# Kernel optimization log

Hardware: AMD Instinct MI355X
Metric: run time of the kernel (lower is better)

Reference implementation:

```python
import jax, jax.numpy as jnp
import numpy as np

GAMMA = 2.0
EPS = 1e-06
LAMBDA_DISTANCE = 1.0
LAMBDA_NORMAL = 0.01
LAMBDA_LAPLACIAN = 0.1
CLS = 1


def vertex_normals(v, f, eps=EPS):
    # v: [N,3], f: [F,3] int. Scatter face normals to vertices, then normalize.
    fv = v[f]  # [F,3,3]
    fn = jnp.cross(fv[:, 1] - fv[:, 0], fv[:, 2] - fv[:, 0])  # [F,3]
    vn = jnp.zeros_like(v)
    vn = vn.at[f[:, 0]].add(fn).at[f[:, 1]].add(fn).at[f[:, 2]].add(fn)
    norm = jnp.maximum(jnp.linalg.norm(vn, axis=-1, keepdims=True), eps)
    return vn / norm


def squared_cdist(a, b):
    # [Na,3] x [Nb,3] -> squared euclidean distances [Na,Nb] (clamped >= 0)
    a2 = jnp.sum(a * a, axis=1)[:, None]
    b2 = jnp.sum(b * b, axis=1)[None, :]
    d2 = a2 + b2 - 2.0 * (a @ b.T)
    return jnp.maximum(d2, 0.0)


def sample_binary_targets(label, v, cls=CLS):
    # Nearest-neighbor grid_sample, align_corners=True, padding zeros.
    # grid = 2*v - 1 -> voxel index = round(v * (size-1)); v[:,0]->W, v[:,1]->H, v[:,2]->D.
    D, H, W = label.shape[2], label.shape[3], label.shape[4]
    ix = jnp.round(v[:, 0] * (W - 1)).astype(jnp.int32)
    iy = jnp.round(v[:, 1] * (H - 1)).astype(jnp.int32)
    iz = jnp.round(v[:, 2] * (D - 1)).astype(jnp.int32)
    inb = (ix >= 0) & (ix < W) & (iy >= 0) & (iy < H) & (iz >= 0) & (iz < D)
    ixc = jnp.clip(ix, 0, W - 1)
    iyc = jnp.clip(iy, 0, H - 1)
    izc = jnp.clip(iz, 0, D - 1)
    vals = (label[0, 0, izc, iyc, ixc] == cls).astype(jnp.float32)
    return jnp.where(inb, vals, 0.0)


def spatial_consistency_loss(rel_pos, targets, gamma=GAMMA, eps=EPS):
    p = jnp.clip(rel_pos, eps, 1.0 - eps)
    pos = targets > 0.5
    pc = jnp.sum(pos).astype(p.dtype)
    tot = jnp.asarray(p.shape[0], p.dtype)
    nc = tot - pc
    alpha = nc / (tot + eps)
    lpos = -alpha * jnp.power(1.0 - p, gamma) * jnp.log(p)
    lneg = -(1.0 - alpha) * jnp.power(p, gamma) * jnp.log(1.0 - p)
    return jnp.sum(jnp.where(pos, lpos, lneg)) / (tot + eps)


def laplacian_uniform(v, f):
    # Uniform mesh Laplacian smoothing: || mean(neighbors) - v ||, averaged.
    i = jnp.concatenate([f[:, 0], f[:, 1], f[:, 2], f[:, 1], f[:, 2], f[:, 0]])
    j = jnp.concatenate([f[:, 1], f[:, 2], f[:, 0], f[:, 0], f[:, 1], f[:, 2]])
    nsum = jnp.zeros_like(v).at[i].add(v[j])
    deg = jnp.zeros((v.shape[0],), v.dtype).at[i].add(1.0)
    lap = nsum / jnp.maximum(deg, 1.0)[:, None] - v
    return jnp.mean(jnp.linalg.norm(lap, axis=1))


def loss_forward(pred_vertices, relative_positions, gt_vertices, pred_faces, gt_faces, label):
    gt_v = jax.lax.stop_gradient(gt_vertices)  # gt comes from label volume; detached in original
    gt_normals = vertex_normals(gt_v, gt_faces)
    # spatial (focal-style) loss
    targets = sample_binary_targets(label, pred_vertices)
    spatial = spatial_consistency_loss(relative_positions, targets)
    # chamfer-style squared surface distance
    d2 = squared_cdist(pred_vertices, gt_v)  # [Np,Ng]
    distance = jnp.mean(jnp.min(d2, axis=1)) + jnp.mean(jnp.min(d2, axis=0))
    # normal consistency vs nearest gt vertex
    pred_normals = vertex_normals(pred_vertices, pred_faces)
    nearest = jnp.argmin(d2, axis=1)
    normal = jnp.mean((pred_normals - gt_normals[nearest]) ** 2)
    # uniform laplacian smoothing
    laplacian = laplacian_uniform(pred_vertices, pred_faces)
    total = spatial + LAMBDA_DISTANCE * distance + LAMBDA_NORMAL * normal + LAMBDA_LAPLACIAN * laplacian
    return total


def setup_inputs() -> dict:
    key = jax.random.key(0)
    k1, k2, k3, k4, k5, k6 = jax.random.split(key, 6)
    Np, Ng = 8192, 12000
    pred_vertices = jax.random.uniform(k1, (Np, 3), dtype=jnp.float32)
    relative_positions = jax.random.uniform(k2, (Np,), dtype=jnp.float32)
    gt_vertices = jax.random.uniform(k3, (Ng, 3), dtype=jnp.float32)
    pred_faces = jax.random.randint(k4, (2 * Np, 3), 0, Np, dtype=jnp.int32)
    gt_faces = jax.random.randint(k5, (2 * Ng, 3), 0, Ng, dtype=jnp.int32)
    label = jax.random.randint(k6, (1, 1, 96, 96, 96), 0, 2, dtype=jnp.int32)
    return {"pred_vertices": pred_vertices, "relative_positions": relative_positions,
            "gt_vertices": gt_vertices, "pred_faces": pred_faces,
            "gt_faces": gt_faces, "label": label}


def reference(pred_vertices, relative_positions, gt_vertices, pred_faces, gt_faces, label):
    return loss_forward(pred_vertices, relative_positions, gt_vertices, pred_faces, gt_faces, label)
```

## Files before the change

### kernel.cpp

```cpp
#include <hip/hip_runtime.h>
#include <math.h>

#define NP 8192
#define NG 12000
#define NFP 16384
#define NFG 24000
#define EPSF 1e-6f

#define GR 16
#define NC (GR*GR*GR)
#define HCELL 0.0625f
#define QL 16

#define FB ((NFG + NFP + 1023) / 1024)
#define D1_BLOCKS (2 + FB)

#define QPBLK 64
#define PQB (NP / QPBLK)
#define GQB ((NG + QPBLK - 1) / QPBLK)
#define D2_BLOCKS (PQB + GQB)

#define CAPP  4608
#define CWCAP 1312

#define FIN_BLOCKS (NP / 256)

static constexpr size_t OFF_STARTP = 0;
static constexpr size_t OFF_STARTG = 16640;
static constexpr size_t OFF_SORTP  = 33280;
static constexpr size_t OFF_SORTG  = 164352;
static constexpr size_t OFF_GTN    = 356352;
static constexpr size_t OFF_PNN    = 500352;
static constexpr size_t OFF_NSUM   = 598656;
static constexpr size_t OFF_DEG    = 696960;
static constexpr size_t OFF_NEAR   = 729728;
static constexpr size_t OFF_ACCUM  = 762496;
static constexpr size_t OFF_DONE   = 762528;
static constexpr size_t ZERO_BYTES = OFF_DONE + 4 - OFF_GTN;

__device__ __forceinline__ int cell_of(float x) {
    int c = (int)(x * (float)GR);
    return min(max(c, 0), GR - 1);
}

__device__ __forceinline__ void build_cells(const float* __restrict__ pts, int n,
                                            unsigned* __restrict__ start,
                                            float4* __restrict__ sorted,
                                            unsigned* h, unsigned* wsum) {
    int t = threadIdx.x;
    int lane = t & 63, wid = t >> 6;
    for (int i = t; i < NC; i += 1024) h[i] = 0u;
    __syncthreads();
    for (int i = t; i < n; i += 1024) {
        int c = (cell_of(pts[3*i+2]) * GR + cell_of(pts[3*i+1])) * GR + cell_of(pts[3*i]);
        atomicAdd(&h[c], 1u);
    }
    __syncthreads();
    unsigned a0 = h[4*t], a1 = h[4*t+1], a2 = h[4*t+2], a3 = h[4*t+3];
    unsigned tsum = a0 + a1 + a2 + a3;
    unsigned x = tsum;
    #pragma unroll
    for (int off = 1; off < 64; off <<= 1) {
        unsigned y = __shfl_up(x, off, 64);
        if (lane >= off) x += y;
    }
    if (lane == 63) wsum[wid] = x;
    __syncthreads();
    if (t < 16) {
        unsigned w = wsum[t];
        #pragma unroll
        for (int off = 1; off < 16; off <<= 1) {
            unsigned y = __shfl_up(w, off, 64);
            if (t >= off) w += y;
        }
        wsum[t] = w;
    }
    __syncthreads();
    unsigned base = (wid ? wsum[wid-1] : 0u) + (x - tsum);
    unsigned e0 = base, e1 = base + a0, e2 = base + a0 + a1, e3 = base + a0 + a1 + a2;
    start[4*t] = e0; start[4*t+1] = e1; start[4*t+2] = e2; start[4*t+3] = e3;
    h[4*t] = e0; h[4*t+1] = e1; h[4*t+2] = e2; h[4*t+3] = e3;
    __syncthreads();
    for (int i = t; i < n; i += 1024) {
        float px = pts[3*i], py = pts[3*i+1], pz = pts[3*i+2];
        int c = (cell_of(pz) * GR + cell_of(py)) * GR + cell_of(px);
        unsigned pos = atomicAdd(&h[c], 1u);
        sorted[pos] = make_float4(px, py, pz, __int_as_float(i));
    }
    if (t == 0) start[NC] = (unsigned)n;
}

__global__ __launch_bounds__(1024) void build_face_kernel(const float* __restrict__ pred,
                                                          const float* __restrict__ gt,
                                                          const int* __restrict__ pf,
                                                          const int* __restrict__ gf,
                                                          unsigned* __restrict__ startP,
                                                          unsigned* __restrict__ startG,
                                                          float4* __restrict__ sortP,
                                                          float4* __restrict__ sortG,
                                                          float* __restrict__ gtn,
                                                          float* __restrict__ pnn,
                                                          float* __restrict__ nsum,
                                                          float* __restrict__ deg) {
    __shared__ unsigned h[NC];
    __shared__ unsigned wsum[16];
    int b = blockIdx.x, t = threadIdx.x;
    if (b == 0) {
        build_cells(pred, NP, startP, sortP, h, wsum);
    } else if (b == 1) {
        build_cells(gt, NG, startG, sortG, h, wsum);
    } else {
        int f = (b - 2) * 1024 + t;
        if (f < NFG) {
            int i0 = gf[3*f], i1 = gf[3*f+1], i2 = gf[3*f+2];
            float ax = gt[3*i0], ay = gt[3*i0+1], az = gt[3*i0+2];
            float bx = gt[3*i1], by = gt[3*i1+1], bz = gt[3*i1+2];
            float cx = gt[3*i2], cy = gt[3*i2+1], cz = gt[3*i2+2];
            float ux = bx-ax, uy = by-ay, uz = bz-az;
            float wx = cx-ax, wy = cy-ay, wz = cz-az;
            float nx = uy*wz - uz*wy, ny = uz*wx - ux*wz, nz = ux*wy - uy*wx;
            atomicAdd(&gtn[3*i0+0], nx); atomicAdd(&gtn[3*i0+1], ny); atomicAdd(&gtn[3*i0+2], nz);
            atomicAdd(&gtn[3*i1+0], nx); atomicAdd(&gtn[3*i1+1], ny); atomicAdd(&gtn[3*i1+2], nz);
            atomicAdd(&gtn[3*i2+0], nx); atomicAdd(&gtn[3*i2+1], ny); atomicAdd(&gtn[3*i2+2], nz);
        } else if (f < NFG + NFP) {
            int u = f - NFG;
            int i0 = pf[3*u], i1 = pf[3*u+1], i2 = pf[3*u+2];
            float ax = pred[3*i0], ay = pred[3*i0+1], az = pred[3*i0+2];
            float bx = pred[3*i1], by = pred[3*i1+1], bz = pred[3*i1+2];
            float cx = pred[3*i2], cy = pred[3*i2+1], cz = pred[3*i2+2];
            float ux = bx-ax, uy = by-ay, uz = bz-az;
            float wx = cx-ax, wy = cy-ay, wz = cz-az;
            float nx = uy*wz - uz*wy, ny = uz*wx - ux*wz, nz = ux*wy - uy*wx;
            atomicAdd(&pnn[3*i0+0], nx); atomicAdd(&pnn[3*i0+1], ny); atomicAdd(&pnn[3*i0+2], nz);
            atomicAdd(&pnn[3*i1+0], nx); atomicAdd(&pnn[3*i1+1], ny); atomicAdd(&pnn[3*i1+2], nz);
            atomicAdd(&pnn[3*i2+0], nx); atomicAdd(&pnn[3*i2+1], ny); atomicAdd(&pnn[3*i2+2], nz);
            atomicAdd(&nsum[3*i0+0], bx+cx); atomicAdd(&nsum[3*i0+1], by+cy); atomicAdd(&nsum[3*i0+2], bz+cz);
            atomicAdd(&nsum[3*i1+0], cx+ax); atomicAdd(&nsum[3*i1+1], cy+ay); atomicAdd(&nsum[3*i1+2], cz+az);
            atomicAdd(&nsum[3*i2+0], ax+bx); atomicAdd(&nsum[3*i2+1], ay+by); atomicAdd(&nsum[3*i2+2], az+bz);
            atomicAdd(&deg[i0], 2.0f); atomicAdd(&deg[i1], 2.0f); atomicAdd(&deg[i2], 2.0f);
        }
    }
}

__device__ __forceinline__ float wave_sum(float x) {
    #pragma unroll
    for (int o = 32; o > 0; o >>= 1) x += __shfl_down(x, o, 64);
    return x;
}

__device__ __forceinline__ unsigned long long u64min(unsigned long long a,
                                                     unsigned long long b) {
    return a < b ? a : b;
}

__device__ __forceinline__ unsigned long long pack_key(float px, float py, float pz,
                                                       float4 q) {
    float ddx = px - q.x, ddy = py - q.y, ddz = pz - q.z;
    float d2 = fmaf(ddx, ddx, fmaf(ddy, ddy, ddz*ddz));
    return ((unsigned long long)__float_as_uint(d2) << 32) |
           (unsigned)__float_as_int(q.w);
}

__device__ unsigned long long group_nn(int lane, float px, float py, float pz,
                                       const float4* __restrict__ Sg,
                                       const unsigned* __restrict__ CSg,
                                       const float4* Sl, const unsigned* CSl,
                                       int c_lo, unsigned p_lo, bool staged) {
    int cx = cell_of(px), cy = cell_of(py), cz = cell_of(pz);
    unsigned long long best = 0xFFFFFFFFFFFFFFFFULL;
    {
        unsigned long long lb = 0xFFFFFFFFFFFFFFFFULL;
        for (int k = lane; k < 27; k += QL) {
            int z = cz + k / 9 - 1, y = cy + (k % 9) / 3 - 1, x = cx + k % 3 - 1;
            if (((unsigned)z < GR) & ((unsigned)y < GR) & ((unsigned)x < GR)) {
                int c = (z * GR + y) * GR + x;
                if (staged) {
                    unsigned s0 = CSl[c - c_lo];
                    unsigned s1 = CSl[c + 1 - c_lo];
                    for (unsigned u = s0; u < s1; ++u)
                        lb = u64min(lb, pack_key(px, py, pz, Sl[u - p_lo]));
                } else {
                    unsigned s0 = CSg[c];
                    unsigned s1 = CSg[c + 1];
                    for (unsigned u = s0; u < s1; ++u)
                        lb = u64min(lb, pack_key(px, py, pz, Sg[u]));
                }
            }
        }
        best = lb;
        #pragma unroll
        for (int m = 1; m < QL; m <<= 1)
            best = u64min(best, (unsigned long long)__shfl_xor((long long)best, m, 64));
        bool covered = (cx - 1 <= 0) & (cx + 1 >= GR - 1) &
                       (cy - 1 <= 0) & (cy + 1 >= GR - 1) &
                       (cz - 1 <= 0) & (cz + 1 >= GR - 1);
        float blo = 1.0e30f;
        if (cx - 1 > 0)      blo = fminf(blo, px - (float)(cx - 1) * HCELL);
        if (cx + 1 < GR - 1) blo = fminf(blo, (float)(cx + 2) * HCELL - px);
        if (cy - 1 > 0)      blo = fminf(blo, py - (float)(cy - 1) * HCELL);
        if (cy + 1 < GR - 1) blo = fminf(blo, (float)(cy + 2) * HCELL - py);
        if (cz - 1 > 0)      blo = fminf(blo, pz - (float)(cz - 1) * HCELL);
        if (cz + 1 < GR - 1) blo = fminf(blo, (float)(cz + 2) * HCELL - pz);
        float bd2 = __uint_as_float((unsigned)(best >> 32));
        if (covered || (bd2 <= blo * blo)) return best;
    }
    for (int r = 2; ; ++r) {
        int w = 2 * r + 1;
        int nrows = w * w;
        int x0 = max(cx - r, 0), x1 = min(cx + r, GR - 1);
        unsigned long long lb = 0xFFFFFFFFFFFFFFFFULL;
        for (int k = lane; k < nrows; k += QL) {
            int z = cz + k / w - r, y = cy + k % w - r;
            if (z >= 0 && z < GR && y >= 0 && y < GR) {
                int rowbase = (z * GR + y) * GR;
                unsigned s0 = CSg[rowbase + x0];
                unsigned s1 = CSg[rowbase + x1 + 1];
                for (unsigned u = s0; u < s1; ++u)
                    lb = u64min(lb, pack_key(px, py, pz, Sg[u]));
            }
        }
        best = u64min(best, lb);
        #pragma unroll
        for (int m = 1; m < QL; m <<= 1)
            best = u64min(best, (unsigned long long)__shfl_xor((long long)best, m, 64));
        bool covered = (cx - r <= 0) & (cx + r >= GR - 1) &
                       (cy - r <= 0) & (cy + r >= GR - 1) &
                       (cz - r <= 0) & (cz + r >= GR - 1);
        if (covered) break;
        float blo = 1.0e30f;
        if (cx - r > 0)      blo = fminf(blo, px - (float)(cx - r) * HCELL);
        if (cx + r < GR - 1) blo = fminf(blo, (float)(cx + r + 1) * HCELL - px);
        if (cy - r > 0)      blo = fminf(blo, py - (float)(cy - r) * HCELL);
        if (cy + r < GR - 1) blo = fminf(blo, (float)(cy + r + 1) * HCELL - py);
        if (cz - r > 0)      blo = fminf(blo, pz - (float)(cz - r) * HCELL);
        if (cz + r < GR - 1) blo = fminf(blo, (float)(cz + r + 1) * HCELL - pz);
        float bd2 = __uint_as_float((unsigned)(best >> 32));
        if (bd2 <= blo * blo) break;
    }
    return best;
}

__global__ __launch_bounds__(1024) void query_kernel(const float4* __restrict__ sortP,
                                                     const float4* __restrict__ sortG,
                                                     const unsigned* __restrict__ startP,
                                                     const unsigned* __restrict__ startG,
                                                     int* __restrict__ nearestIdx,
                                                     float* __restrict__ accum) {
    __shared__ float4 lpts[CAPP];
    __shared__ unsigned lcs[CWCAP];
    __shared__ float qacc;
    __shared__ int s_info[4];
    int b = blockIdx.x, t = threadIdx.x;

    bool is_pred = (b < PQB);
    const float4*   Q  = is_pred ? sortP  : sortG;
    const float4*   S  = is_pred ? sortG  : sortP;
    const unsigned* CS = is_pred ? startG : startP;
    int qbase = (is_pred ? b : (b - PQB)) * QPBLK;
    int nq = min(QPBLK, (is_pred ? NP : NG) - qbase);

    if (t == 0) {
        qacc = 0.0f;
        float4 qf = Q[qbase], ql = Q[qbase + nq - 1];
        int z_lo = cell_of(qf.z), z_hi = cell_of(ql.z);
        int c_lo  = max(z_lo - 1, 0) * (GR * GR);
        int c_end = min(z_hi + 2, GR) * (GR * GR);
        int cw = c_end - c_lo + 1;
        unsigned p_lo = CS[c_lo], p_hi = CS[c_end];
        int np = (int)(p_hi - p_lo);
        bool ok = (cw <= CWCAP) && (np <= CAPP);
        s_info[0] = c_lo; s_info[1] = (int)p_lo; s_info[2] = np;
        s_info[3] = ok ? cw : -cw;
    }
    __syncthreads();
    int c_lo = s_info[0];
    unsigned p_lo = (unsigned)s_info[1];
    int np = s_info[2];
    int cw = s_info[3];
    bool staged = (cw > 0);
    if (staged) {
        for (int i = t; i < np; i += 1024) lpts[i] = S[p_lo + i];
        for (int i = t; i < cw; i += 1024) lcs[i]  = CS[c_lo + i];
    }
    __syncthreads();

    int lane = t & (QL - 1), group = t >> 4;
    float r0 = 0.0f;
    if (group < nq) {
        int qid = qbase + group;
        float4 P = Q[qid];
        unsigned long long key = group_nn(lane, P.x, P.y, P.z, S, CS,
                                          lpts, lcs, c_lo, p_lo, staged);
        if (lane == 0) {
            r0 = __uint_as_float((unsigned)(key >> 32));
            if (is_pred)
                nearestIdx[__float_as_int(P.w)] = (int)(unsigned)(key & 0xffffffffu);
        }
    }
    r0 = wave_sum(r0);
    if ((t & 63) == 0) atomicAdd(&qacc, r0);
    __syncthreads();
    if (t == 0) atomicAdd(&accum[is_pred ? 0 : 6], qacc);
}

__global__ __launch_bounds__(256) void finish_kernel(const float* __restrict__ pred,
                                                     const float* __restrict__ relpos,
                                                     const int* __restrict__ label,
                                                     const float* __restrict__ pnn,
                                                     const float* __restrict__ gtn,
                                                     const float* __restrict__ nsum,
                                                     const float* __restrict__ deg,
                                                     const int* __restrict__ nearestIdx,
                                                     float* __restrict__ accum,
                                                     unsigned* __restrict__ done,
                                                     float* __restrict__ out) {
    int v = blockIdx.x * 256 + threadIdx.x;
    float px = pred[3*v], py = pred[3*v+1], pz = pred[3*v+2];
    int nearest = nearestIdx[v];

    float ax = pnn[3*v], ay = pnn[3*v+1], az = pnn[3*v+2];
    float an = fmaxf(sqrtf(ax*ax + ay*ay + az*az), EPSF);
    float gx = gtn[3*nearest], gy = gtn[3*nearest+1], gz = gtn[3*nearest+2];
    float gn = fmaxf(sqrtf(gx*gx + gy*gy + gz*gz), EPSF);
    float nx = ax/an - gx/gn, ny = ay/an - gy/gn, nz = az/an - gz/gn;
    float sse = nx*nx + ny*ny + nz*nz;

    float d = fmaxf(deg[v], 1.0f);
    float lx = nsum[3*v]/d - px, ly = nsum[3*v+1]/d - py, lz = nsum[3*v+2]/d - pz;
    float lapn = sqrtf(lx*lx + ly*ly + lz*lz);

    int ix = (int)rintf(px * 95.0f), iy = (int)rintf(py * 95.0f), iz = (int)rintf(pz * 95.0f);
    bool inb = (ix >= 0) & (ix < 96) & (iy >= 0) & (iy < 96) & (iz >= 0) & (iz < 96);
    int ixc = min(max(ix, 0), 95), iyc = min(max(iy, 0), 95), izc = min(max(iz, 0), 95);
    bool pos = inb && (label[(izc*96 + iyc)*96 + ixc] == 1);

    float p = fminf(fmaxf(relpos[v], EPSF), 1.0f - EPSF);
    float om = 1.0f - p;
    float pcnt = 0.0f, sx = 0.0f, sy = 0.0f;
    if (pos) { pcnt = 1.0f; sx = om*om*logf(p); }
    else     { sy = p*p*logf(om); }

    float r1 = wave_sum(sse), r2 = wave_sum(lapn), r3 = wave_sum(pcnt);
    float r4 = wave_sum(sx),  r5 = wave_sum(sy);
    __shared__ float bsum[5];
    __shared__ bool isLast;
    if (threadIdx.x < 5) bsum[threadIdx.x] = 0.0f;
    __syncthreads();
    if ((threadIdx.x & 63) == 0) {
        atomicAdd(&bsum[0], r1); atomicAdd(&bsum[1], r2); atomicAdd(&bsum[2], r3);
        atomicAdd(&bsum[3], r4); atomicAdd(&bsum[4], r5);
    }
    __syncthreads();
    if (threadIdx.x == 0) {
        atomicAdd(&accum[1], bsum[0]); atomicAdd(&accum[2], bsum[1]);
        atomicAdd(&accum[3], bsum[2]); atomicAdd(&accum[4], bsum[3]);
        atomicAdd(&accum[5], bsum[4]);
        __threadfence();
        unsigned prev = atomicAdd(done, 1u);
        isLast = (prev == FIN_BLOCKS - 1);
    }
    __syncthreads();
    if (isLast && threadIdx.x == 0) {
        __threadfence();
        float sum_row = __hip_atomic_load(&accum[0], __ATOMIC_RELAXED, __HIP_MEMORY_SCOPE_AGENT);
        float sse_t   = __hip_atomic_load(&accum[1], __ATOMIC_RELAXED, __HIP_MEMORY_SCOPE_AGENT);
        float lap_t   = __hip_atomic_load(&accum[2], __ATOMIC_RELAXED, __HIP_MEMORY_SCOPE_AGENT);
        float pc      = __hip_atomic_load(&accum[3], __ATOMIC_RELAXED, __HIP_MEMORY_SCOPE_AGENT);
        float SX      = __hip_atomic_load(&accum[4], __ATOMIC_RELAXED, __HIP_MEMORY_SCOPE_AGENT);
        float SY      = __hip_atomic_load(&accum[5], __ATOMIC_RELAXED, __HIP_MEMORY_SCOPE_AGENT);
        float sum_col = __hip_atomic_load(&accum[6], __ATOMIC_RELAXED, __HIP_MEMORY_SCOPE_AGENT);
        float tot = (float)NP;
        float alpha = (tot - pc) / (tot + EPSF);
        float spatial = (-alpha * SX - (1.0f - alpha) * SY) / (tot + EPSF);
        float distance = sum_row / (float)NP + sum_col / (float)NG;
        float normal = sse_t / (float)(NP * 3);
        float lapm = lap_t / (float)NP;
        out[0] = spatial + 1.0f * distance + 0.01f * normal + 0.1f * lapm;
    }
}

extern "C" void kernel_launch(void* const* d_in, const int* in_sizes, int n_in,
                              void* d_out, int out_size, void* d_ws, size_t ws_size,
                              hipStream_t stream) {
    const float* pred   = (const float*)d_in[0];
    const float* relpos = (const float*)d_in[1];
    const float* gt     = (const float*)d_in[2];
    const int*   pfaces = (const int*)d_in[3];
    const int*   gfaces = (const int*)d_in[4];
    const int*   label  = (const int*)d_in[5];
    float* out = (float*)d_out;

    char* ws = (char*)d_ws;
    unsigned* startP  = (unsigned*)(ws + OFF_STARTP);
    unsigned* startG  = (unsigned*)(ws + OFF_STARTG);
    float4*   sortP   = (float4*)(ws + OFF_SORTP);
    float4*   sortG   = (float4*)(ws + OFF_SORTG);
    float*    gtn     = (float*)(ws + OFF_GTN);
    float*    pnn     = (float*)(ws + OFF_PNN);
    float*    nsum    = (float*)(ws + OFF_NSUM);
    float*    deg     = (float*)(ws + OFF_DEG);
    int*      nearest = (int*)(ws + OFF_NEAR);
    float*    accum   = (float*)(ws + OFF_ACCUM);
    unsigned* done    = (unsigned*)(ws + OFF_DONE);

    hipMemsetAsync(ws + OFF_GTN, 0, ZERO_BYTES, stream);
    hipLaunchKernelGGL(build_face_kernel, dim3(D1_BLOCKS), dim3(1024), 0, stream,
                       pred, gt, pfaces, gfaces, startP, startG, sortP, sortG,
                       gtn, pnn, nsum, deg);
    hipLaunchKernelGGL(query_kernel, dim3(D2_BLOCKS), dim3(1024), 0, stream,
                       sortP, sortG, startP, startG, nearest, accum);
    hipLaunchKernelGGL(finish_kernel, dim3(FIN_BLOCKS), dim3(256), 0, stream,
                       pred, relpos, label, pnn, gtn, nsum, deg, nearest,
                       accum, done, out);
}
```

Baseline: 131.2 us.

## Replace float atomic scatters with CSR vertex-to-face gather and drop memset

Builds per-vertex incidence lists (CSR) for pred and gt faces in shared-memory histogram blocks in the first kernel. Gt vertex normals are then gathered in extra blocks of the query kernel, and pred normals and Laplacian sums are gathered inside the finish kernel. This removes the global float atomics and the memset launch, and makes the sums deterministic. In exchange, two single blocks must process all face indices serially in the build kernel, which risks becoming a long serial stage.

```diff
diff --git a/kernel.cpp b/kernel.cpp
--- a/kernel.cpp
+++ b/kernel.cpp
@@ -12,31 +12,31 @@
 #define HCELL 0.0625f
 #define QL 16
 
-#define FB ((NFG + NFP + 1023) / 1024)
-#define D1_BLOCKS (2 + FB)
+#define D1_BLOCKS 4
 
 #define QPBLK 64
 #define PQB (NP / QPBLK)
 #define GQB ((NG + QPBLK - 1) / QPBLK)
-#define D2_BLOCKS (PQB + GQB)
+#define GGB ((NG + 1023) / 1024)
+#define D2_BLOCKS (PQB + GQB + GGB)
 
 #define CAPP  4608
 #define CWCAP 1312
 
 #define FIN_BLOCKS (NP / 256)
 
-static constexpr size_t OFF_STARTP = 0;
-static constexpr size_t OFF_STARTG = 16640;
-static constexpr size_t OFF_SORTP  = 33280;
-static constexpr size_t OFF_SORTG  = 164352;
-static constexpr size_t OFF_GTN    = 356352;
-static constexpr size_t OFF_PNN    = 500352;
-static constexpr size_t OFF_NSUM   = 598656;
-static constexpr size_t OFF_DEG    = 696960;
-static constexpr size_t OFF_NEAR   = 729728;
-static constexpr size_t OFF_ACCUM  = 762496;
-static constexpr size_t OFF_DONE   = 762528;
-static constexpr size_t ZERO_BYTES = OFF_DONE + 4 - OFF_GTN;
+static constexpr size_t OFF_STARTP  = 0;
+static constexpr size_t OFF_STARTG  = 16640;
+static constexpr size_t OFF_SORTP   = 33280;
+static constexpr size_t OFF_SORTG   = 164352;
+static constexpr size_t OFF_GTN     = 356352;
+static constexpr size_t OFF_ISTARTP = 500352;
+static constexpr size_t OFF_IRECP   = 533136;
+static constexpr size_t OFF_ISTARTG = 729744;
+static constexpr size_t OFF_IRECG   = 777760;
+static constexpr size_t OFF_NEAR    = 1065760;
+static constexpr size_t OFF_ACCUM   = 1098528;
+static constexpr size_t OFF_DONE    = 1098560;
 
 __device__ __forceinline__ int cell_of(float x) {
     int c = (int)(x * (float)GR);
@@ -90,55 +90,85 @@
     if (t == 0) start[NC] = (unsigned)n;
 }
 
-__global__ __launch_bounds__(1024) void build_face_kernel(const float* __restrict__ pred,
-                                                          const float* __restrict__ gt,
-                                                          const int* __restrict__ pf,
-                                                          const int* __restrict__ gf,
-                                                          unsigned* __restrict__ startP,
-                                                          unsigned* __restrict__ startG,
-                                                          float4* __restrict__ sortP,
-                                                          float4* __restrict__ sortG,
-                                                          float* __restrict__ gtn,
-                                                          float* __restrict__ pnn,
-                                                          float* __restrict__ nsum,
-                                                          float* __restrict__ deg) {
-    __shared__ unsigned h[NC];
+template<int K>
+__device__ void build_csr(const int* __restrict__ f, int nf, int nv,
+                          unsigned* __restrict__ istart,
+                          unsigned* __restrict__ irec,
+                          unsigned* h, unsigned* wsum) {
+    int t = threadIdx.x;
+    int lane = t & 63, wid = t >> 6;
+    const int nbins = K * 1024;
+    for (int i = t; i < nbins; i += 1024) h[i] = 0u;
+    __syncthreads();
+    for (int i = t; i < 3 * nf; i += 1024) atomicAdd(&h[f[i]], 1u);
+    __syncthreads();
+    unsigned a[K];
+    unsigned tsum = 0;
+    #pragma unroll
+    for (int k = 0; k < K; ++k) { a[k] = h[K*t + k]; tsum += a[k]; }
+    unsigned x = tsum;
+    #pragma unroll
+    for (int off = 1; off < 64; off <<= 1) {
+        unsigned y = __shfl_up(x, off, 64);
+        if (lane >= off) x += y;
+    }
+    if (lane == 63) wsum[wid] = x;
+    __syncthreads();
+    if (t < 16) {
+        unsigned w = wsum[t];
+        #pragma unroll
+        for (int off = 1; off < 16; off <<= 1) {
+            unsigned y = __shfl_up(w, off, 64);
+            if (t >= off) w += y;
+        }
+        wsum[t] = w;
+    }
+    __syncthreads();
+    unsigned run = (wid ? wsum[wid-1] : 0u) + (x - tsum);
+    #pragma unroll
+    for (int k = 0; k < K; ++k) {
+        int idx = K*t + k;
+        if (idx <= nv) istart[idx] = run;
+        h[idx] = run;
+        run += a[k];
+    }
+    if (t == 0) istart[nv] = (unsigned)(3 * nf);
+    __syncthreads();
+    for (int i = t; i < nf; i += 1024) {
+        int i0 = f[3*i], i1 = f[3*i+1], i2 = f[3*i+2];
+        unsigned p0 = atomicAdd(&h[i0], 1u); irec[p0] = ((unsigned)i << 2) | 0u;
+        unsigned p1 = atomicAdd(&h[i1], 1u); irec[p1] = ((unsigned)i << 2) | 1u;
+        unsigned p2 = atomicAdd(&h[i2], 1u); irec[p2] = ((unsigned)i << 2) | 2u;
+    }
+}
+
+__global__ __launch_bounds__(1024) void build_kernel(const float* __restrict__ pred,
+                                                     const float* __restrict__ gt,
+                                                     const int* __restrict__ pf,
+                                                     const int* __restrict__ gf,
+                                                     unsigned* __restrict__ startP,
+                                                     unsigned* __restrict__ startG,
+                                                     float4* __restrict__ sortP,
+                                                     float4* __restrict__ sortG,
+                                                     unsigned* __restrict__ istartP,
+                                                     unsigned* __restrict__ irecP,
+                                                     unsigned* __restrict__ istartG,
+                                                     unsigned* __restrict__ irecG,
+                                                     float* __restrict__ accum,
+                                                     unsigned* __restrict__ done) {
+    __shared__ unsigned h[12288];
     __shared__ unsigned wsum[16];
     int b = blockIdx.x, t = threadIdx.x;
     if (b == 0) {
         build_cells(pred, NP, startP, sortP, h, wsum);
     } else if (b == 1) {
         build_cells(gt, NG, startG, sortG, h, wsum);
+    } else if (b == 2) {
+        if (t < 8) accum[t] = 0.0f;
+        if (t == 8) *done = 0u;
+        build_csr<8>(pf, NFP, NP, istartP, irecP, h, wsum);
     } else {
-        int f = (b - 2) * 1024 + t;
-        if (f < NFG) {
-            int i0 = gf[3*f], i1 = gf[3*f+1], i2 = gf[3*f+2];
-            float ax = gt[3*i0], ay = gt[3*i0+1], az = gt[3*i0+2];
-            float bx = gt[3*i1], by = gt[3*i1+1], bz = gt[3*i1+2];
-            float cx = gt[3*i2], cy = gt[3*i2+1], cz = gt[3*i2+2];
-            float ux = bx-ax, uy = by-ay, uz = bz-az;
-            float wx = cx-ax, wy = cy-ay, wz = cz-az;
-            float nx = uy*wz - uz*wy, ny = uz*wx - ux*wz, nz = ux*wy - uy*wx;
-            atomicAdd(&gtn[3*i0+0], nx); atomicAdd(&gtn[3*i0+1], ny); atomicAdd(&gtn[3*i0+2], nz);
-            atomicAdd(&gtn[3*i1+0], nx); atomicAdd(&gtn[3*i1+1], ny); atomicAdd(&gtn[3*i1+2], nz);
-            atomicAdd(&gtn[3*i2+0], nx); atomicAdd(&gtn[3*i2+1], ny); atomicAdd(&gtn[3*i2+2], nz);
-        } else if (f < NFG + NFP) {
-            int u = f - NFG;
-            int i0 = pf[3*u], i1 = pf[3*u+1], i2 = pf[3*u+2];
-            float ax = pred[3*i0], ay = pred[3*i0+1], az = pred[3*i0+2];
-            float bx = pred[3*i1], by = pred[3*i1+1], bz = pred[3*i1+2];
-            float cx = pred[3*i2], cy = pred[3*i2+1], cz = pred[3*i2+2];
-            float ux = bx-ax, uy = by-ay, uz = bz-az;
-            float wx = cx-ax, wy = cy-ay, wz = cz-az;
-            float nx = uy*wz - uz*wy, ny = uz*wx - ux*wz, nz = ux*wy - uy*wx;
-            atomicAdd(&pnn[3*i0+0], nx); atomicAdd(&pnn[3*i0+1], ny); atomicAdd(&pnn[3*i0+2], nz);
-            atomicAdd(&pnn[3*i1+0], nx); atomicAdd(&pnn[3*i1+1], ny); atomicAdd(&pnn[3*i1+2], nz);
-            atomicAdd(&pnn[3*i2+0], nx); atomicAdd(&pnn[3*i2+1], ny); atomicAdd(&pnn[3*i2+2], nz);
-            atomicAdd(&nsum[3*i0+0], bx+cx); atomicAdd(&nsum[3*i0+1], by+cy); atomicAdd(&nsum[3*i0+2], bz+cz);
-            atomicAdd(&nsum[3*i1+0], cx+ax); atomicAdd(&nsum[3*i1+1], cy+ay); atomicAdd(&nsum[3*i1+2], cz+az);
-            atomicAdd(&nsum[3*i2+0], ax+bx); atomicAdd(&nsum[3*i2+1], ay+by); atomicAdd(&nsum[3*i2+2], az+bz);
-            atomicAdd(&deg[i0], 2.0f); atomicAdd(&deg[i1], 2.0f); atomicAdd(&deg[i2], 2.0f);
-        }
+        build_csr<12>(gf, NFG, NG, istartG, irecG, h, wsum);
     }
 }
 
@@ -240,17 +270,42 @@
     return best;
 }
 
-__global__ __launch_bounds__(1024) void query_kernel(const float4* __restrict__ sortP,
-                                                     const float4* __restrict__ sortG,
-                                                     const unsigned* __restrict__ startP,
-                                                     const unsigned* __restrict__ startG,
-                                                     int* __restrict__ nearestIdx,
-                                                     float* __restrict__ accum) {
+__global__ __launch_bounds__(1024) void query_gather_kernel(const float* __restrict__ gt,
+                                                            const int* __restrict__ gf,
+                                                            const float4* __restrict__ sortP,
+                                                            const float4* __restrict__ sortG,
+                                                            const unsigned* __restrict__ startP,
+                                                            const unsigned* __restrict__ startG,
+                                                            const unsigned* __restrict__ istartG,
+                                                            const unsigned* __restrict__ irecG,
+                                                            float* __restrict__ gtn,
+                                                            int* __restrict__ nearestIdx,
+                                                            float* __restrict__ accum) {
     __shared__ float4 lpts[CAPP];
     __shared__ unsigned lcs[CWCAP];
     __shared__ float qacc;
     __shared__ int s_info[4];
     int b = blockIdx.x, t = threadIdx.x;
+
+    if (b >= PQB + GQB) {
+        int v = (b - PQB - GQB) * 1024 + t;
+        if (v < NG) {
+            unsigned s = istartG[v], e = istartG[v+1];
+            float nx = 0.f, ny = 0.f, nz = 0.f;
+            for (unsigned u = s; u < e; ++u) {
+                int fid = (int)(irecG[u] >> 2);
+                int i0 = gf[3*fid], i1 = gf[3*fid+1], i2 = gf[3*fid+2];
+                float ax = gt[3*i0], ay = gt[3*i0+1], az = gt[3*i0+2];
+                float bx = gt[3*i1], by = gt[3*i1+1], bz = gt[3*i1+2];
+                float cx = gt[3*i2], cy = gt[3*i2+1], cz = gt[3*i2+2];
+                float ux = bx-ax, uy = by-ay, uz = bz-az;
+                float wx = cx-ax, wy = cy-ay, wz = cz-az;
+                nx += uy*wz - uz*wy; ny += uz*wx - ux*wz; nz += ux*wy - uy*wx;
+            }
+            gtn[3*v] = nx; gtn[3*v+1] = ny; gtn[3*v+2] = nz;
+        }
+        return;
+    }
 
     bool is_pred = (b < PQB);
     const float4*   Q  = is_pred ? sortP  : sortG;
@@ -306,10 +361,10 @@
 __global__ __launch_bounds__(256) void finish_kernel(const float* __restrict__ pred,
                                                      const float* __restrict__ relpos,
                                                      const int* __restrict__ label,
-                                                     const float* __restrict__ pnn,
+                                                     const int* __restrict__ pf,
+                                                     const unsigned* __restrict__ istartP,
+                                                     const unsigned* __restrict__ irecP,
                                                      const float* __restrict__ gtn,
-                                                     const float* __restrict__ nsum,
-                                                     const float* __restrict__ deg,
                                                      const int* __restrict__ nearestIdx,
                                                      float* __restrict__ accum,
                                                      unsigned* __restrict__ done,
@@ -318,15 +373,32 @@
     float px = pred[3*v], py = pred[3*v+1], pz = pred[3*v+2];
     int nearest = nearestIdx[v];
 
-    float ax = pnn[3*v], ay = pnn[3*v+1], az = pnn[3*v+2];
-    float an = fmaxf(sqrtf(ax*ax + ay*ay + az*az), EPSF);
+    unsigned s = istartP[v], e = istartP[v+1];
+    float ax_ = 0.f, ay_ = 0.f, az_ = 0.f;
+    float nsx = 0.f, nsy = 0.f, nsz = 0.f;
+    for (unsigned u = s; u < e; ++u) {
+        unsigned rec = irecP[u];
+        int fid = (int)(rec >> 2), slot = (int)(rec & 3u);
+        int i0 = pf[3*fid], i1 = pf[3*fid+1], i2 = pf[3*fid+2];
+        float Ax = pred[3*i0], Ay = pred[3*i0+1], Az = pred[3*i0+2];
+        float Bx = pred[3*i1], By = pred[3*i1+1], Bz = pred[3*i1+2];
+        float Cx = pred[3*i2], Cy = pred[3*i2+1], Cz = pred[3*i2+2];
+        float ux = Bx-Ax, uy = By-Ay, uz = Bz-Az;
+        float wx = Cx-Ax, wy = Cy-Ay, wz = Cz-Az;
+        ax_ += uy*wz - uz*wy; ay_ += uz*wx - ux*wz; az_ += ux*wy - uy*wx;
+        if (slot == 0)      { nsx += Bx+Cx; nsy += By+Cy; nsz += Bz+Cz; }
+        else if (slot == 1) { nsx += Cx+Ax; nsy += Cy+Ay; nsz += Cz+Az; }
+        else                { nsx += Ax+Bx; nsy += Ay+By; nsz += Az+Bz; }
+    }
+    float d = fmaxf(2.0f * (float)(e - s), 1.0f);
+
+    float an = fmaxf(sqrtf(ax_*ax_ + ay_*ay_ + az_*az_), EPSF);
     float gx = gtn[3*nearest], gy = gtn[3*nearest+1], gz = gtn[3*nearest+2];
     float gn = fmaxf(sqrtf(gx*gx + gy*gy + gz*gz), EPSF);
-    float nx = ax/an - gx/gn, ny = ay/an - gy/gn, nz = az/an - gz/gn;
+    float nx = ax_/an - gx/gn, ny = ay_/an - gy/gn, nz = az_/an - gz/gn;
     float sse = nx*nx + ny*ny + nz*nz;
 
-    float d = fmaxf(deg[v], 1.0f);
-    float lx = nsum[3*v]/d - px, ly = nsum[3*v+1]/d - py, lz = nsum[3*v+2]/d - pz;
+    float lx = nsx/d - px, ly = nsy/d - py, lz = nsz/d - pz;
     float lapn = sqrtf(lx*lx + ly*ly + lz*lz);
 
     int ix = (int)rintf(px * 95.0f), iy = (int)rintf(py * 95.0f), iz = (int)rintf(pz * 95.0f);
@@ -396,20 +468,21 @@
     float4*   sortP   = (float4*)(ws + OFF_SORTP);
     float4*   sortG   = (float4*)(ws + OFF_SORTG);
     float*    gtn     = (float*)(ws + OFF_GTN);
-    float*    pnn     = (float*)(ws + OFF_PNN);
-    float*    nsum    = (float*)(ws + OFF_NSUM);
-    float*    deg     = (float*)(ws + OFF_DEG);
+    unsigned* istartP = (unsigned*)(ws + OFF_ISTARTP);
+    unsigned* irecP   = (unsigned*)(ws + OFF_IRECP);
+    unsigned* istartG = (unsigned*)(ws + OFF_ISTARTG);
+    unsigned* irecG   = (unsigned*)(ws + OFF_IRECG);
     int*      nearest = (int*)(ws + OFF_NEAR);
     float*    accum   = (float*)(ws + OFF_ACCUM);
     unsigned* done    = (unsigned*)(ws + OFF_DONE);
 
-    hipMemsetAsync(ws + OFF_GTN, 0, ZERO_BYTES, stream);
-    hipLaunchKernelGGL(build_face_kernel, dim3(D1_BLOCKS), dim3(1024), 0, stream,
+    hipLaunchKernelGGL(build_kernel, dim3(D1_BLOCKS), dim3(1024), 0, stream,
                        pred, gt, pfaces, gfaces, startP, startG, sortP, sortG,
-                       gtn, pnn, nsum, deg);
-    hipLaunchKernelGGL(query_kernel, dim3(D2_BLOCKS), dim3(1024), 0, stream,
-                       sortP, sortG, startP, startG, nearest, accum);
+                       istartP, irecP, istartG, irecG, accum, done);
+    hipLaunchKernelGGL(query_gather_kernel, dim3(D2_BLOCKS), dim3(1024), 0, stream,
+                       gt, gfaces, sortP, sortG, startP, startG,
+                       istartG, irecG, gtn, nearest, accum);
     hipLaunchKernelGGL(finish_kernel, dim3(FIN_BLOCKS), dim3(256), 0, stream,
-                       pred, relpos, label, pnn, gtn, nsum, deg, nearest,
-                       accum, done, out);
-}
+                       pred, relpos, label, pfaces, istartP, irecP,
+                       gtn, nearest, accum, done, out);
+}
```

Result: slower. 173.5 us (+32.3%).
